# Performance work log

Hardware: AMD Instinct MI355X
Metric: run time of the kernel (lower is better)

Reference implementation:

```python
import jax, jax.numpy as jnp
import numpy as np


def setup_inputs() -> dict:
    key = jax.random.key(0)
    k1, k2 = jax.random.split(key)
    token_inputs = jax.random.normal(k1, (4, 2048, 4096), dtype=jnp.float32)
    w_gate = jax.random.normal(k2, (4096, 64), dtype=jnp.float32)
    return {"token_inputs": token_inputs, "w_gate": w_gate, "expert_capacity": 40}


def reference(token_inputs, w_gate, expert_capacity):
    # Gating: [b, n, d] @ [d, e] -> [b, n, e]
    router_logits = jnp.einsum('bnd,de->bne', token_inputs, w_gate)

    # Router z-loss: mean of squared logsumexp over experts.
    z_loss = jnp.mean(jax.nn.logsumexp(router_logits, axis=-1) ** 2)

    router_probs = jax.nn.softmax(router_logits, axis=-1)
    num_experts = router_probs.shape[-1]

    # Top-1 (Switch) routing.
    expert_index = jnp.argmax(router_probs, axis=-1)          # [b, n]
    expert_gate = jnp.max(router_probs, axis=-1)              # [b, n]
    expert_mask = jax.nn.one_hot(expert_index, num_experts,
                                 dtype=router_probs.dtype)    # [b, n, e]

    # Load-balancing auxiliary loss.
    density = jnp.mean(expert_mask, axis=1)                   # [b, e] dispatch fraction
    density_proxy = jnp.mean(router_probs, axis=1)            # [b, e] mean prob
    aux_loss = jnp.mean(density * density_proxy) * (num_experts ** 2)

    # Capacity assignment via cumulative sum over tokens (0-based slot index).
    position_in_expert = (jnp.cumsum(expert_mask, axis=1) - 1.0) * expert_mask  # [b, n, e]
    within_capacity = (position_in_expert < expert_capacity).astype(router_probs.dtype) * expert_mask

    pos_idx = position_in_expert.astype(jnp.int32)            # [b, n, e]
    # Dispatch: one-hot over capacity slots, zeroed for dropped tokens. [b, n, e, c]
    dispatch_tensor = within_capacity[..., None] * jax.nn.one_hot(
        pos_idx, expert_capacity, dtype=router_probs.dtype)
    # Combine: dispatch scaled by the router gate probability.
    combine_tensor = dispatch_tensor * expert_gate[:, :, None, None]

    return dispatch_tensor, combine_tensor, aux_loss, z_loss
```

## Files before the change

kernel.cpp:

```cpp
#include <hip/hip_runtime.h>
#include <stdint.h>

#define B_    4
#define N_    2048
#define D_    4096
#define E_    64
#define TOKENS (B_ * N_)
#define KT    32
#define TTOK  32

__global__ __launch_bounds__(128) void k_gemm(const float* __restrict__ A,
                                              const float* __restrict__ W,
                                              float* __restrict__ P,
                                              int kchunk) {
    __shared__ float As[KT][TTOK + 4];
    __shared__ float Ws[KT][E_];

    const int tid  = threadIdx.x;
    const int tt   = blockIdx.x;
    const int kc   = blockIdx.y;
    const int tok0 = tt * TTOK;
    const int kbase = kc * kchunk;

    const int t0 = (tid & 7) * 4;
    const int e0 = (tid >> 3) * 4;

    float acc[4][4] = {{0.f}};

    for (int kt = 0; kt < kchunk; kt += KT) {
        {
            const int kk = tid & 31;
            const int tb = tid >> 5;
            const float* ga = A + (size_t)tok0 * D_ + (size_t)(kbase + kt) + kk;
            #pragma unroll
            for (int i = 0; i < 8; ++i) {
                const int tok = tb + i * 4;
                As[kk][tok] = ga[(size_t)tok * D_];
            }
        }
        {
            const int e4 = (tid & 15) * 4;
            const int kb = tid >> 4;
            #pragma unroll
            for (int i = 0; i < 4; ++i) {
                const int kk = kb + i * 8;
                const float4 v = *reinterpret_cast<const float4*>(
                    &W[(size_t)(kbase + kt + kk) * E_ + e4]);
                *reinterpret_cast<float4*>(&Ws[kk][e4]) = v;
            }
        }
        __syncthreads();

        #pragma unroll
        for (int kk = 0; kk < KT; ++kk) {
            const float4 a = *reinterpret_cast<const float4*>(&As[kk][t0]);
            const float4 b = *reinterpret_cast<const float4*>(&Ws[kk][e0]);
            acc[0][0] += a.x * b.x; acc[0][1] += a.x * b.y;
            acc[0][2] += a.x * b.z; acc[0][3] += a.x * b.w;
            acc[1][0] += a.y * b.x; acc[1][1] += a.y * b.y;
            acc[1][2] += a.y * b.z; acc[1][3] += a.y * b.w;
            acc[2][0] += a.z * b.x; acc[2][1] += a.z * b.y;
            acc[2][2] += a.z * b.z; acc[2][3] += a.z * b.w;
            acc[3][0] += a.w * b.x; acc[3][1] += a.w * b.y;
            acc[3][2] += a.w * b.z; acc[3][3] += a.w * b.w;
        }
        __syncthreads();
    }

    float* base = P + ((size_t)kc * TOKENS + tok0) * E_;
    #pragma unroll
    for (int i = 0; i < 4; ++i) {
        float4 v = make_float4(acc[i][0], acc[i][1], acc[i][2], acc[i][3]);
        *reinterpret_cast<float4*>(&base[(size_t)(t0 + i) * E_ + e0]) = v;
    }
}

__global__ __launch_bounds__(256) void k_softmax(const float* __restrict__ P,
                                                 int* __restrict__ idx,
                                                 float* __restrict__ gate,
                                                 float* __restrict__ probsum,
                                                 float* __restrict__ zbins,
                                                 int ks) {
    const int tid  = threadIdx.x;
    const int wid  = tid >> 6;
    const int lane = tid & 63;
    const int tok  = blockIdx.x * 4 + wid;

    float l = 0.f;
    for (int kc = 0; kc < ks; ++kc)
        l += P[((size_t)kc * TOKENS + tok) * E_ + lane];

    float m = l; int mi = lane;
    #pragma unroll
    for (int off = 32; off > 0; off >>= 1) {
        const float om = __shfl_down(m, off);
        const int   oi = __shfl_down(mi, off);
        if (om > m || (om == m && oi < mi)) { m = om; mi = oi; }
    }
    m  = __shfl(m, 0);
    mi = __shfl(mi, 0);

    const float p = __expf(l - m);
    float s = p;
    #pragma unroll
    for (int off = 32; off > 0; off >>= 1) s += __shfl_down(s, off);
    s = __shfl(s, 0);

    const float prob = p / s;

    __shared__ float pacc[4][E_];
    __shared__ float zv[4];
    pacc[wid][lane] = prob;
    if (lane == 0) {
        const float lse = m + logf(s);
        zv[wid]   = lse * lse;
        idx[tok]  = mi;
        gate[tok] = 1.0f / s;
    }
    __syncthreads();

    if (tid < E_) {
        const float ps = pacc[0][tid] + pacc[1][tid] + pacc[2][tid] + pacc[3][tid];
        const int b = (blockIdx.x * 4) / N_;
        atomicAdd(&probsum[b * E_ + tid], ps);
    }
    if (tid == 0)
        atomicAdd(&zbins[blockIdx.x & 63], zv[0] + zv[1] + zv[2] + zv[3]);
}

__global__ __launch_bounds__(64) void k_pos(const int* __restrict__ idx,
                                            int* __restrict__ pos,
                                            int* __restrict__ counts) {
    const int b = blockIdx.x >> 6;
    const int e = blockIdx.x & 63;
    const int lane = threadIdx.x;
    const int* ib = idx + b * N_;
    int running = 0;
    for (int step = 0; step < N_ / 64; ++step) {
        const int t = step * 64 + lane;
        const bool match = (ib[t] == e);
        const unsigned long long mask = __ballot(match);
        if (match)
            pos[b * N_ + t] = running + __popcll(mask & ((1ull << lane) - 1ull));
        running += __popcll(mask);
    }
    if (lane == 0) counts[b * E_ + e] = running;
}

__global__ __launch_bounds__(256) void k_loss(const int* __restrict__ counts,
                                              const float* __restrict__ probsum,
                                              const float* __restrict__ zbins,
                                              float* __restrict__ out_aux,
                                              float* __restrict__ out_z) {
    __shared__ float red[256];
    const int tid = threadIdx.x;
    red[tid] = (float)counts[tid] * probsum[tid];
    __syncthreads();
    for (int off = 128; off > 0; off >>= 1) {
        if (tid < off) red[tid] += red[tid + off];
        __syncthreads();
    }
    if (tid == 0) {
        *out_aux = red[0] * (1.0f / 262144.0f);
        float z = 0.f;
        for (int i = 0; i < 64; ++i) z += zbins[i];
        *out_z = z / (float)TOKENS;
    }
}

__global__ __launch_bounds__(256) void k_scatter(const int* __restrict__ idx,
                                                 const int* __restrict__ pos,
                                                 const float* __restrict__ gate,
                                                 float* __restrict__ out,
                                                 int C, size_t half) {
    const int t = blockIdx.x * 256 + threadIdx.x;
    if (t >= TOKENS) return;
    const int p = pos[t];
    if (p < C) {
        const size_t off = (size_t)t * E_ * C + (size_t)idx[t] * C + p;
        out[off] = 1.0f;
        out[half + off] = gate[t];
    }
}

extern "C" void kernel_launch(void* const* d_in, const int* in_sizes, int n_in,
                              void* d_out, int out_size, void* d_ws, size_t ws_size,
                              hipStream_t stream) {
    const float* A = (const float*)d_in[0];
    const float* W = (const float*)d_in[1];
    float* out = (float*)d_out;

    const size_t half = ((size_t)out_size - 2) / 2;
    const int C = (int)(half / ((size_t)TOKENS * E_));

    int ks = 8;
    auto need = [](int k) {
        return ((size_t)k * TOKENS * E_ + 3 * TOKENS + 2 * B_ * E_ + 64) * 4;
    };
    while (ks > 1 && need(ks) > ws_size) ks >>= 1;
    const int kchunk = D_ / ks;

    float* P = (float*)d_ws;
    size_t off = (size_t)ks * TOKENS * E_;
    int*   idx     = (int*)(P + off);   off += TOKENS;
    int*   pos     = (int*)(P + off);   off += TOKENS;
    float* gate    = P + off;           off += TOKENS;
    float* probsum = P + off;           off += B_ * E_;
    float* zbins   = P + off;           off += 64;
    int*   counts  = (int*)(P + off);   off += B_ * E_;

    hipMemsetAsync(d_out, 0, (size_t)out_size * sizeof(float), stream);
    hipMemsetAsync(probsum, 0, (B_ * E_ + 64) * sizeof(float), stream);

    k_gemm<<<dim3(TOKENS / TTOK, ks), 128, 0, stream>>>(A, W, P, kchunk);
    k_softmax<<<TOKENS / 4, 256, 0, stream>>>(P, idx, gate, probsum, zbins, ks);
    k_pos<<<B_ * E_, 64, 0, stream>>>(idx, pos, counts);
    k_loss<<<1, 256, 0, stream>>>(counts, probsum, zbins,
                                  out + 2 * half, out + 2 * half + 1);
    k_scatter<<<(TOKENS + 255) / 256, 256, 0, stream>>>(idx, pos, gate, out, C, half);
}
```

Baseline: 332.2 us.

## Retile gating GEMM with vectorized A loads and fuse position, scatter and loss kernels

The gating GEMM now uses 64-token tiles with 256 threads, loads A as float4 along K and pads the W shared tile, which is meant to cut global load instructions and improve reuse. The position, scatter and aux-loss kernels are merged into one kernel that writes dispatch/combine entries directly. The z-loss and aux-loss are now accumulated with atomics straight into the output. This drops two launches and the intermediate pos/counts buffers. The trade-offs are transposing stores into shared memory with possible bank conflicts, and float atomic summation order that is no longer deterministic.

Result: slower. 342.0 us (+2.9%).

```diff
diff --git a/kernel.cpp b/kernel.cpp
--- a/kernel.cpp
+++ b/kernel.cpp
@@ -7,47 +7,47 @@
 #define E_    64
 #define TOKENS (B_ * N_)
 #define KT    32
-#define TTOK  32
+#define TM    64
 
-__global__ __launch_bounds__(128) void k_gemm(const float* __restrict__ A,
+__global__ __launch_bounds__(256) void k_gemm(const float* __restrict__ A,
                                               const float* __restrict__ W,
                                               float* __restrict__ P,
                                               int kchunk) {
-    __shared__ float As[KT][TTOK + 4];
-    __shared__ float Ws[KT][E_];
+    __shared__ float As[KT][TM + 4];
+    __shared__ float Ws[KT][E_ + 4];
 
-    const int tid  = threadIdx.x;
-    const int tt   = blockIdx.x;
-    const int kc   = blockIdx.y;
-    const int tok0 = tt * TTOK;
-    const int kbase = kc * kchunk;
+    const int tid   = threadIdx.x;
+    const int tok0  = blockIdx.x * TM;
+    const int kbase = blockIdx.y * kchunk;
 
-    const int t0 = (tid & 7) * 4;
-    const int e0 = (tid >> 3) * 4;
+    const int t0 = (tid >> 4) * 4;
+    const int e0 = (tid & 15) * 4;
+
+    const int a_kf = (tid & 7) * 4;
+    const int a_t  = tid >> 3;
+    const int w_e  = (tid & 15) * 4;
+    const int w_k  = tid >> 4;
 
     float acc[4][4] = {{0.f}};
 
     for (int kt = 0; kt < kchunk; kt += KT) {
-        {
-            const int kk = tid & 31;
-            const int tb = tid >> 5;
-            const float* ga = A + (size_t)tok0 * D_ + (size_t)(kbase + kt) + kk;
-            #pragma unroll
-            for (int i = 0; i < 8; ++i) {
-                const int tok = tb + i * 4;
-                As[kk][tok] = ga[(size_t)tok * D_];
-            }
+        const float* gA = A + (size_t)tok0 * D_ + (size_t)(kbase + kt);
+        #pragma unroll
+        for (int it = 0; it < 2; ++it) {
+            const int tok = a_t + it * 32;
+            const float4 v = *reinterpret_cast<const float4*>(
+                gA + (size_t)tok * D_ + a_kf);
+            As[a_kf + 0][tok] = v.x;
+            As[a_kf + 1][tok] = v.y;
+            As[a_kf + 2][tok] = v.z;
+            As[a_kf + 3][tok] = v.w;
         }
-        {
-            const int e4 = (tid & 15) * 4;
-            const int kb = tid >> 4;
-            #pragma unroll
-            for (int i = 0; i < 4; ++i) {
-                const int kk = kb + i * 8;
-                const float4 v = *reinterpret_cast<const float4*>(
-                    &W[(size_t)(kbase + kt + kk) * E_ + e4]);
-                *reinterpret_cast<float4*>(&Ws[kk][e4]) = v;
-            }
+        const float* gW = W + (size_t)(kbase + kt) * E_;
+        #pragma unroll
+        for (int it = 0; it < 2; ++it) {
+            const int kk = w_k + it * 16;
+            const float4 v = *reinterpret_cast<const float4*>(gW + kk * E_ + w_e);
+            *reinterpret_cast<float4*>(&Ws[kk][w_e]) = v;
         }
         __syncthreads();
 
@@ -67,10 +67,10 @@
         __syncthreads();
     }
 
-    float* base = P + ((size_t)kc * TOKENS + tok0) * E_;
+    float* base = P + ((size_t)blockIdx.y * TOKENS + tok0) * E_;
     #pragma unroll
     for (int i = 0; i < 4; ++i) {
-        float4 v = make_float4(acc[i][0], acc[i][1], acc[i][2], acc[i][3]);
+        const float4 v = make_float4(acc[i][0], acc[i][1], acc[i][2], acc[i][3]);
         *reinterpret_cast<float4*>(&base[(size_t)(t0 + i) * E_ + e0]) = v;
     }
 }
@@ -79,7 +79,7 @@
                                                  int* __restrict__ idx,
                                                  float* __restrict__ gate,
                                                  float* __restrict__ probsum,
-                                                 float* __restrict__ zbins,
+                                                 float* __restrict__ out_z,
                                                  int ks) {
     const int tid  = threadIdx.x;
     const int wid  = tid >> 6;
@@ -106,11 +106,9 @@
     for (int off = 32; off > 0; off >>= 1) s += __shfl_down(s, off);
     s = __shfl(s, 0);
 
-    const float prob = p / s;
-
     __shared__ float pacc[4][E_];
     __shared__ float zv[4];
-    pacc[wid][lane] = prob;
+    pacc[wid][lane] = p / s;
     if (lane == 0) {
         const float lse = m + logf(s);
         zv[wid]   = lse * lse;
@@ -125,62 +123,40 @@
         atomicAdd(&probsum[b * E_ + tid], ps);
     }
     if (tid == 0)
-        atomicAdd(&zbins[blockIdx.x & 63], zv[0] + zv[1] + zv[2] + zv[3]);
+        atomicAdd(out_z, (zv[0] + zv[1] + zv[2] + zv[3]) * (1.0f / (float)TOKENS));
 }
 
-__global__ __launch_bounds__(64) void k_pos(const int* __restrict__ idx,
-                                            int* __restrict__ pos,
-                                            int* __restrict__ counts) {
+__global__ __launch_bounds__(64) void k_posloss(const int* __restrict__ idx,
+                                                const float* __restrict__ gate,
+                                                const float* __restrict__ probsum,
+                                                float* __restrict__ out,
+                                                float* __restrict__ out_aux,
+                                                int C, size_t half) {
     const int b = blockIdx.x >> 6;
     const int e = blockIdx.x & 63;
     const int lane = threadIdx.x;
-    const int* ib = idx + b * N_;
+    const int*   ib = idx  + b * N_;
+    const float* gb = gate + b * N_;
+    float* ob = out + (size_t)b * N_ * E_ * C;
+
     int running = 0;
     for (int step = 0; step < N_ / 64; ++step) {
         const int t = step * 64 + lane;
         const bool match = (ib[t] == e);
         const unsigned long long mask = __ballot(match);
-        if (match)
-            pos[b * N_ + t] = running + __popcll(mask & ((1ull << lane) - 1ull));
+        if (match) {
+            const int p = running + __popcll(mask & ((1ull << lane) - 1ull));
+            if (p < C) {
+                const size_t off = (size_t)t * E_ * C + (size_t)e * C + p;
+                ob[off] = 1.0f;
+                ob[half + off] = gb[t];
+            }
+        }
         running += __popcll(mask);
     }
-    if (lane == 0) counts[b * E_ + e] = running;
-}
-
-__global__ __launch_bounds__(256) void k_loss(const int* __restrict__ counts,
-                                              const float* __restrict__ probsum,
-                                              const float* __restrict__ zbins,
-                                              float* __restrict__ out_aux,
-                                              float* __restrict__ out_z) {
-    __shared__ float red[256];
-    const int tid = threadIdx.x;
-    red[tid] = (float)counts[tid] * probsum[tid];
-    __syncthreads();
-    for (int off = 128; off > 0; off >>= 1) {
-        if (tid < off) red[tid] += red[tid + off];
-        __syncthreads();
-    }
-    if (tid == 0) {
-        *out_aux = red[0] * (1.0f / 262144.0f);
-        float z = 0.f;
-        for (int i = 0; i < 64; ++i) z += zbins[i];
-        *out_z = z / (float)TOKENS;
-    }
-}
-
-__global__ __launch_bounds__(256) void k_scatter(const int* __restrict__ idx,
-                                                 const int* __restrict__ pos,
-                                                 const float* __restrict__ gate,
-                                                 float* __restrict__ out,
-                                                 int C, size_t half) {
-    const int t = blockIdx.x * 256 + threadIdx.x;
-    if (t >= TOKENS) return;
-    const int p = pos[t];
-    if (p < C) {
-        const size_t off = (size_t)t * E_ * C + (size_t)idx[t] * C + p;
-        out[off] = 1.0f;
-        out[half + off] = gate[t];
-    }
+    if (lane == 0)
+        atomicAdd(out_aux,
+                  (float)running * probsum[b * E_ + e] * (1.0f / 262144.0f));
 }
 
 extern "C" void kernel_launch(void* const* d_in, const int* in_sizes, int n_in,
@@ -195,7 +171,7 @@
 
     int ks = 8;
     auto need = [](int k) {
-        return ((size_t)k * TOKENS * E_ + 3 * TOKENS + 2 * B_ * E_ + 64) * 4;
+        return ((size_t)k * TOKENS * E_ + 2 * TOKENS + B_ * E_) * 4;
     };
     while (ks > 1 && need(ks) > ws_size) ks >>= 1;
     const int kchunk = D_ / ks;
@@ -203,19 +179,16 @@
     float* P = (float*)d_ws;
     size_t off = (size_t)ks * TOKENS * E_;
     int*   idx     = (int*)(P + off);   off += TOKENS;
-    int*   pos     = (int*)(P + off);   off += TOKENS;
     float* gate    = P + off;           off += TOKENS;
     float* probsum = P + off;           off += B_ * E_;
-    float* zbins   = P + off;           off += 64;
-    int*   counts  = (int*)(P + off);   off += B_ * E_;
+
+    float* out_aux = out + 2 * half;
+    float* out_z   = out + 2 * half + 1;
 
     hipMemsetAsync(d_out, 0, (size_t)out_size * sizeof(float), stream);
-    hipMemsetAsync(probsum, 0, (B_ * E_ + 64) * sizeof(float), stream);
+    hipMemsetAsync(probsum, 0, B_ * E_ * sizeof(float), stream);
 
-    k_gemm<<<dim3(TOKENS / TTOK, ks), 128, 0, stream>>>(A, W, P, kchunk);
-    k_softmax<<<TOKENS / 4, 256, 0, stream>>>(P, idx, gate, probsum, zbins, ks);
-    k_pos<<<B_ * E_, 64, 0, stream>>>(idx, pos, counts);
-    k_loss<<<1, 256, 0, stream>>>(counts, probsum, zbins,
-                                  out + 2 * half, out + 2 * half + 1);
-    k_scatter<<<(TOKENS + 255) / 256, 256, 0, stream>>>(idx, pos, gate, out, C, half);
+    k_gemm<<<dim3(TOKENS / TM, ks), 256, 0, stream>>>(A, W, P, kchunk);
+    k_softmax<<<TOKENS / 4, 256, 0, stream>>>(P, idx, gate, probsum, out_z, ks);
+    k_posloss<<<B_ * E_, 64, 0, stream>>>(idx, gate, probsum, out, out_aux, C, half);
 }
```
